# Kernel tuning notes

Measured on AMD Instinct MI355X. Metric: run time of the kernel, lower is better.

The kernel has to match this reference:

```python
import jax, jax.numpy as jnp
import numpy as np

VOCAB, EMB, HID, OUT = 32000, 512, 1024, 512
B, S = 64, 256


def setup_inputs() -> dict:
    key = jax.random.key(0)
    ks = jax.random.split(key, 16)
    def xavier(k, shape):
        bound = np.sqrt(6.0 / (shape[0] + shape[1]))
        return jax.random.uniform(k, shape, jnp.float32, -bound, bound)
    return {
        "tokens": jax.random.randint(ks[0], (B, S), 0, VOCAB),
        "emb": jax.random.normal(ks[1], (VOCAB, EMB), jnp.float32) * 0.02,
        "W_xi": xavier(ks[2], (EMB, HID)),
        "W_xf": xavier(ks[3], (EMB, HID)),
        "W_xo": xavier(ks[4], (EMB, HID)),
        "W_xc": xavier(ks[5], (EMB, HID)),
        "W_hi": xavier(ks[6], (HID, HID)),
        "W_hf": xavier(ks[7], (HID, HID)),
        "W_ho": xavier(ks[8], (HID, HID)),
        "W_hc": xavier(ks[9], (HID, HID)),
        "W_hy": xavier(ks[10], (HID, OUT)),
        "b_i": jnp.zeros((HID,), jnp.float32),
        "b_f": jnp.zeros((HID,), jnp.float32),
        "b_o": jnp.zeros((HID,), jnp.float32),
        "b_c": jnp.zeros((HID,), jnp.float32),
        "b_hy": jnp.zeros((OUT,), jnp.float32),
    }


def reference(tokens, emb, W_xi, W_xf, W_xo, W_xc, W_hi, W_hf, W_ho, W_hc,
              W_hy, b_i, b_f, b_o, b_c, b_hy):
    # Embedding lookup for all timesteps (dropout is identity at inference).
    x = emb[tokens]  # [B, S, E]
    # Precompute input-to-gate projections in one batched GEMM per gate.
    gx_i = jnp.einsum('bse,eh->bsh', x, W_xi) + b_i
    gx_f = jnp.einsum('bse,eh->bsh', x, W_xf) + b_f
    gx_o = jnp.einsum('bse,eh->bsh', x, W_xo) + b_o
    gx_c = jnp.einsum('bse,eh->bsh', x, W_xc) + b_c
    # Time-major stacked gates: [S, B, 4, H]
    g = jnp.stack([gx_i, gx_f, gx_o, gx_c], axis=2).transpose(1, 0, 2, 3)

    h0 = jnp.zeros((tokens.shape[0], W_hi.shape[0]), x.dtype)
    c0 = jnp.zeros_like(h0)

    def step(carry, g_t):
        h, c = carry
        i = jax.nn.sigmoid(g_t[:, 0] + h @ W_hi)
        f = jax.nn.sigmoid(g_t[:, 1] + h @ W_hf)
        o = jax.nn.sigmoid(g_t[:, 2] + h @ W_ho)
        cc = jnp.tanh(g_t[:, 3] + h @ W_hc)
        c = f * c + i * cc
        h = o * jnp.tanh(c)
        return (h, c), None

    (h, c), _ = jax.lax.scan(step, (h0, c0), g)
    return h @ W_hy + b_hy  # [B, OUT]
```

## Files before the change

### kernel.cpp

```cpp
#include <hip/hip_runtime.h>
#include <hip/hip_bf16.h>

#define EMBN   512
#define HIDN   1024
#define OUTN   512
#define BBN    64
#define SSN    256
#define NBLK   256
#define PSTR   20

typedef __attribute__((ext_vector_type(8))) short bf16x8;
typedef __attribute__((ext_vector_type(4))) float f32x4;
typedef __attribute__((ext_vector_type(4))) int int4v;
typedef unsigned short us;
typedef unsigned long long ull;

static __device__ __forceinline__ us f2bf(float x) {
  unsigned int u = __float_as_uint(x);
  unsigned int r = (u + 0x7fffu + ((u >> 16) & 1u)) >> 16;
  return (us)r;
}
static __device__ __forceinline__ float bf2f(us u) {
  unsigned int v = ((unsigned int)u) << 16;
  return __uint_as_float(v);
}

__global__ void pack_w(const float* __restrict__ wxi, const float* __restrict__ wxf,
                       const float* __restrict__ wxo, const float* __restrict__ wxc,
                       const float* __restrict__ whi, const float* __restrict__ whf,
                       const float* __restrict__ who, const float* __restrict__ whc,
                       us* __restrict__ Whip, us* __restrict__ Wlop) {
  int idx = blockIdx.x * 256 + threadIdx.x;
  int lane = idx & 63;
  int kt   = (idx >> 6) % 48;
  int j    = idx / (48 * 64);
  int q = lane & 15, g = q >> 2, r = q & 3;
  int hd = 4 * j + r;
  int kb = kt * 32 + ((lane >> 4) << 3);
  const float* wx = (g == 0) ? wxi : (g == 1) ? wxf : (g == 2) ? wxo : wxc;
  const float* wh = (g == 0) ? whi : (g == 1) ? whf : (g == 2) ? who : whc;
  long obase = (long)idx * 8;
  #pragma unroll
  for (int jj = 0; jj < 8; ++jj) {
    int k = kb + jj;
    float v = (k < EMBN) ? wx[(long)k * HIDN + hd] : wh[(long)(k - EMBN) * HIDN + hd];
    us hi = f2bf(v);
    us lo = f2bf(v - bf2f(hi));
    Whip[obase + jj] = hi;
    Wlop[obase + jj] = lo;
  }
}

__global__ void pack_x(const int* __restrict__ tokens, const float* __restrict__ emb,
                       us* __restrict__ Xhi, us* __restrict__ Xlo) {
  int idx = blockIdx.x * 256 + threadIdx.x;
  int k = idx & 511;
  int b = (idx >> 9) & 63;
  int t = idx >> 15;
  int tok = tokens[b * SSN + t];
  float v = emb[(long)tok * EMBN + k];
  us hi = f2bf(v);
  Xhi[idx] = hi;
  Xlo[idx] = f2bf(v - bf2f(hi));
}

#define XISS(A, c) { _Pragma("unroll") for (int q = 0; q < 4; ++q) { \
      A[2*q]   = *(const bf16x8*)(xh + (((c)*4 + q) << 5)); \
      A[2*q+1] = *(const bf16x8*)(xl + (((c)*4 + q) << 5)); } }
#define XCON(A, c) { _Pragma("unroll") for (int q = 0; q < 4; ++q) { \
      const int kt = (c)*4 + q; \
      bf16x8 w0 = *(const bf16x8*)(WHi + (kt << 9) + (lane << 3)); \
      bf16x8 w1 = *(const bf16x8*)(WLo + (kt << 9) + (lane << 3)); \
      accA = __builtin_amdgcn_mfma_f32_16x16x32_bf16(w0, A[2*q],   accA, 0, 0, 0); \
      accB = __builtin_amdgcn_mfma_f32_16x16x32_bf16(w0, A[2*q+1], accB, 0, 0, 0); \
      accC = __builtin_amdgcn_mfma_f32_16x16x32_bf16(w1, A[2*q],   accC, 0, 0, 0); } }
#define HISS(A, c) { _Pragma("unroll") for (int q = 0; q < 4; ++q) { \
      A[2*q]   = *(const bf16x8*)(hh + (((c)*4 + q) << 5)); \
      A[2*q+1] = *(const bf16x8*)(hl + (((c)*4 + q) << 5)); } }
#define HCON(A, c) { _Pragma("unroll") for (int q = 0; q < 4; ++q) { \
      const int kt = 16 + (c)*4 + q; \
      bf16x8 w0 = *(const bf16x8*)(WHi + (kt << 9) + (lane << 3)); \
      bf16x8 w1 = *(const bf16x8*)(WLo + (kt << 9) + (lane << 3)); \
      accA = __builtin_amdgcn_mfma_f32_16x16x32_bf16(w0, A[2*q],   accA, 0, 0, 0); \
      accB = __builtin_amdgcn_mfma_f32_16x16x32_bf16(w0, A[2*q+1], accB, 0, 0, 0); \
      accC = __builtin_amdgcn_mfma_f32_16x16x32_bf16(w1, A[2*q],   accC, 0, 0, 0); } }

__launch_bounds__(256, 1)
__global__ void lstm_persist(const us* __restrict__ Whip, const us* __restrict__ Wlop,
                             const us* __restrict__ Xhi, const us* __restrict__ Xlo,
                             us* Hhi, us* Hlo, float* hfin, int* flags,
                             const float* __restrict__ biP, const float* __restrict__ bfP,
                             const float* __restrict__ boP, const float* __restrict__ bcP,
                             int K) {
  extern __shared__ char smem[];
  us* WHi = (us*)smem;
  us* WLo = WHi + 24576;
  float* preact = (float*)(smem + 98304);

  const int j = blockIdx.x, tid = threadIdx.x;
  const int wv = tid >> 6, lane = tid & 63;
  const int Km = K - 1;
  const bool ROT = (K != 256);

  {
    const uint4* shi = (const uint4*)(Whip + (long)j * 24576);
    const uint4* slo = (const uint4*)(Wlop + (long)j * 24576);
    uint4* dhi = (uint4*)WHi;
    uint4* dlo = (uint4*)WLo;
    for (int i = tid; i < 3072; i += 256) { dhi[i] = shi[i]; dlo[i] = slo[i]; }
  }
  const int gb = tid >> 2, gr = tid & 3;
  const float bi_r = biP[4 * j + gr], bf_r = bfP[4 * j + gr];
  const float bo_r = boP[4 * j + gr], bc_r = bcP[4 * j + gr];
  float c_reg = 0.f;

  const int mrow = (wv << 4) + (lane & 15);
  const int kj = (lane >> 4) << 3;
  const int p0 = (lane >> 4) << 2;
  int* const flagsP = flags + (wv << 8);
  __syncthreads();

  f32x4 accA = {0.f, 0.f, 0.f, 0.f};
  f32x4 accB = {0.f, 0.f, 0.f, 0.f};
  f32x4 accC = {0.f, 0.f, 0.f, 0.f};

  {
    const us* xh = Xhi + (mrow << 9) + kj;
    const us* xl = Xlo + (mrow << 9) + kj;
    bf16x8 XA[8], XB[8];
    XISS(XA, 0) XISS(XB, 1)
    __builtin_amdgcn_sched_barrier(0);
    XCON(XA, 0) XISS(XA, 2)
    __builtin_amdgcn_sched_barrier(0);
    XCON(XB, 1) XISS(XB, 3)
    __builtin_amdgcn_sched_barrier(0);
    XCON(XA, 2) XCON(XB, 3)
  }

  #pragma unroll 1
  for (int t = 0; t < SSN; ++t) {
    if (t > 0) {
      if (ROT && (t & Km) == 0)
        __builtin_amdgcn_fence(__ATOMIC_ACQUIRE, "agent");

      {
        const int* fp = flagsP + (lane << 2);
        int4v f;
        for (;;) {
          asm volatile("global_load_dwordx4 %0, %1, off sc0 sc1\n\t"
                       "s_waitcnt vmcnt(0)"
                       : "=&v"(f) : "v"(fp) : "memory");
          if (!__any((f.x < t) | (f.y < t) | (f.z < t) | (f.w < t))) break;
          __builtin_amdgcn_s_sleep(2);
        }
      }

      const int cur = t & Km;
      const us* hh = Hhi + (((long)cur * BBN + mrow) << 10) + kj;
      const us* hl = Hlo + (((long)cur * BBN + mrow) << 10) + kj;
      bf16x8 HA[8], HB[8], HC[8], HD[8];
      HISS(HA, 0) HISS(HB, 1) HISS(HC, 2) HISS(HD, 3)
      __builtin_amdgcn_sched_barrier(0);
      HCON(HA, 0) HISS(HA, 4)
      __builtin_amdgcn_sched_barrier(0);
      HCON(HB, 1) HISS(HB, 5)
      __builtin_amdgcn_sched_barrier(0);
      HCON(HC, 2) HISS(HC, 6)
      __builtin_amdgcn_sched_barrier(0);
      HCON(HD, 3) HISS(HD, 7)
      __builtin_amdgcn_sched_barrier(0);
      HCON(HA, 4) HCON(HB, 5) HCON(HC, 6) HCON(HD, 7)
    }

    {
      f32x4 acc = accA + accB;
      acc = acc + accC;
      *(f32x4*)(preact + mrow * PSTR + p0) = acc;
    }

    {
      float pi = preact[gb * PSTR + gr]      + bi_r;
      float pf = preact[gb * PSTR + 4 + gr]  + bf_r;
      float po = preact[gb * PSTR + 8 + gr]  + bo_r;
      float pc = preact[gb * PSTR + 12 + gr] + bc_r;
      float vi = 1.f / (1.f + expf(-pi));
      float vf = 1.f / (1.f + expf(-pf));
      float vo = 1.f / (1.f + expf(-po));
      float vc = tanhf(pc);
      c_reg = vf * c_reg + vi * vc;
      float h = vo * tanhf(c_reg);

      if (t == SSN - 1) {
        hfin[(gb << 10) + 4 * j + gr] = h;
      } else {
        us hh_ = f2bf(h);
        us hl_ = f2bf(h - bf2f(hh_));
        unsigned int hpair = (unsigned int)hh_ | ((unsigned int)hl_ << 16);
        const int base = lane & ~3;
        unsigned int g0 = (unsigned int)__shfl((int)hpair, base);
        unsigned int g1 = (unsigned int)__shfl((int)hpair, base + 1);
        unsigned int g2 = (unsigned int)__shfl((int)hpair, base + 2);
        unsigned int g3 = (unsigned int)__shfl((int)hpair, base + 3);
        unsigned int hi01 = (g0 & 0xffffu) | (g1 << 16);
        unsigned int hi23 = (g2 & 0xffffu) | (g3 << 16);
        unsigned int lo01 = (g0 >> 16)     | (g1 & 0xffff0000u);
        unsigned int lo23 = (g2 >> 16)     | (g3 & 0xffff0000u);
        ull hiq = ((ull)hi23 << 32) | (ull)hi01;
        ull loq = ((ull)lo23 << 32) | (ull)lo01;

        const long nxt = (long)((t + 1) & Km);
        if (gr == 0) {
          __hip_atomic_store((ull*)(Hhi + ((nxt * BBN + gb) << 10) + 4 * j), hiq,
                             __ATOMIC_RELAXED, __HIP_MEMORY_SCOPE_AGENT);
          __hip_atomic_store((ull*)(Hlo + ((nxt * BBN + gb) << 10) + 4 * j), loq,
                             __ATOMIC_RELAXED, __HIP_MEMORY_SCOPE_AGENT);
        }

        const us* xh = Xhi + ((long)(t + 1) << 15) + (mrow << 9) + kj;
        const us* xl = Xlo + ((long)(t + 1) << 15) + (mrow << 9) + kj;
        bf16x8 XA[8], XB[8];
        XISS(XA, 0) XISS(XB, 1)
        asm volatile("s_waitcnt vmcnt(0)" ::: "memory");
        if (lane == 0)
          __hip_atomic_store(&flagsP[j], t + 1,
                             __ATOMIC_RELAXED, __HIP_MEMORY_SCOPE_AGENT);
        __builtin_amdgcn_sched_barrier(0);
        accA = {0.f, 0.f, 0.f, 0.f};
        accB = {0.f, 0.f, 0.f, 0.f};
        accC = {0.f, 0.f, 0.f, 0.f};
        XCON(XA, 0) XISS(XA, 2)
        __builtin_amdgcn_sched_barrier(0);
        XCON(XB, 1) XISS(XB, 3)
        __builtin_amdgcn_sched_barrier(0);
        XCON(XA, 2) XCON(XB, 3)
      }
    }
  }
}

__global__ void out_gemm(const float* __restrict__ hfin, const float* __restrict__ Why,
                         const float* __restrict__ bhy, float* __restrict__ out) {
  int b = blockIdx.x, n = threadIdx.x;
  const float* h = hfin + (b << 10);
  float acc = 0.f;
  #pragma unroll 8
  for (int k = 0; k < HIDN; ++k) acc = fmaf(h[k], Why[(k << 9) + n], acc);
  out[(b << 9) + n] = acc + bhy[n];
}

extern "C" void kernel_launch(void* const* d_in, const int* in_sizes, int n_in,
                              void* d_out, int out_size, void* d_ws, size_t ws_size,
                              hipStream_t stream) {
  const int*   tokens = (const int*)d_in[0];
  const float* emb    = (const float*)d_in[1];
  const float* Wxi    = (const float*)d_in[2];
  const float* Wxf    = (const float*)d_in[3];
  const float* Wxo    = (const float*)d_in[4];
  const float* Wxc    = (const float*)d_in[5];
  const float* Whi_   = (const float*)d_in[6];
  const float* Whf    = (const float*)d_in[7];
  const float* Who    = (const float*)d_in[8];
  const float* Whc    = (const float*)d_in[9];
  const float* Why    = (const float*)d_in[10];
  const float* bi     = (const float*)d_in[11];
  const float* bfv    = (const float*)d_in[12];
  const float* bo     = (const float*)d_in[13];
  const float* bc     = (const float*)d_in[14];
  const float* bhy    = (const float*)d_in[15];
  float* outp = (float*)d_out;

  char* ws = (char*)d_ws;
  size_t off = 0;
  auto carve = [&](size_t bytes) -> void* {
    void* p = ws + off;
    off += (bytes + 255) & ~(size_t)255;
    return p;
  };
  us*    Whip = (us*)carve(12582912);
  us*    Wlop = (us*)carve(12582912);
  us*    Xhi  = (us*)carve(16777216);
  us*    Xlo  = (us*)carve(16777216);
  float* hfin = (float*)carve(262144);
  int*   flags = (int*)carve(4096);

  size_t rem = (ws_size > off) ? (ws_size - off) : 0;
  int K = 256;
  while (K > 8 && (size_t)2 * (size_t)K * 131072 + 512 > rem) K >>= 1;
  if ((size_t)2 * (size_t)K * 131072 + 512 > rem) {
    (void)hipMemsetAsync(d_out, 0, (size_t)out_size * 4, stream);
    return;
  }
  us* Hhi = (us*)carve((size_t)K * 131072);
  us* Hlo = (us*)carve((size_t)K * 131072);

  (void)hipMemsetAsync(flags, 0, 4096, stream);

  pack_w<<<3072, 256, 0, stream>>>(Wxi, Wxf, Wxo, Wxc, Whi_, Whf, Who, Whc, Whip, Wlop);
  pack_x<<<32768, 256, 0, stream>>>(tokens, emb, Xhi, Xlo);

  (void)hipFuncSetAttribute((const void*)lstm_persist,
                            hipFuncAttributeMaxDynamicSharedMemorySize, 103424);
  lstm_persist<<<NBLK, 256, 103424, stream>>>(Whip, Wlop, Xhi, Xlo, Hhi, Hlo,
                                              hfin, flags, bi, bfv, bo, bc, K);
  out_gemm<<<BBN, OUTN, 0, stream>>>(hfin, Why, bhy, outp);
}
```

Baseline: 2.821 ms.

## Replace per-step flag polling with sentinel-tagged hidden-state data polling

Removes the separate flags array and its spin loop. Consumers now load the hidden-state tiles directly and re-poll only when they see an all-ones sentinel, which the hidden buffers are memset to before launch. Producers no longer need a vmcnt wait plus a flag store after writing h. This saves a round trip on the recurrent critical path. It relies on a valid bf16 pair never equalling 0xFFFFFFFF (NaN pattern), and on the max check over lanes x and z catching partially written tiles. When the buffer ring wraps, slots are re-marked with sentinels, which adds extra stores and a wait.

```diff
diff --git a/kernel.cpp b/kernel.cpp
--- a/kernel.cpp
+++ b/kernel.cpp
@@ -11,7 +11,7 @@
 
 typedef __attribute__((ext_vector_type(8))) short bf16x8;
 typedef __attribute__((ext_vector_type(4))) float f32x4;
-typedef __attribute__((ext_vector_type(4))) int int4v;
+typedef __attribute__((ext_vector_type(4))) unsigned int u32x4;
 typedef unsigned short us;
 typedef unsigned long long ull;
 
@@ -74,9 +74,39 @@
       accA = __builtin_amdgcn_mfma_f32_16x16x32_bf16(w0, A[2*q],   accA, 0, 0, 0); \
       accB = __builtin_amdgcn_mfma_f32_16x16x32_bf16(w0, A[2*q+1], accB, 0, 0, 0); \
       accC = __builtin_amdgcn_mfma_f32_16x16x32_bf16(w1, A[2*q],   accC, 0, 0, 0); } }
-#define HISS(A, c) { _Pragma("unroll") for (int q = 0; q < 4; ++q) { \
-      A[2*q]   = *(const bf16x8*)(hh + (((c)*4 + q) << 5)); \
-      A[2*q+1] = *(const bf16x8*)(hl + (((c)*4 + q) << 5)); } }
+
+#define HLD(A, S, c) { _Pragma("unroll") for (int q = 0; q < 4; ++q) { \
+      const int ct = (c)*4 + q; \
+      u32x4 rh = *(const u32x4*)(hh + (ct << 5)); \
+      u32x4 rl = *(const u32x4*)(hl + (ct << 5)); \
+      A[2*q]   = *(bf16x8*)&rh; \
+      A[2*q+1] = *(bf16x8*)&rl; \
+      unsigned int m0 = rh.x > rh.z ? rh.x : rh.z; \
+      unsigned int m1 = rl.x > rl.z ? rl.x : rl.z; \
+      S[q] = m0 > m1 ? m0 : m1; } }
+#define HRLD(A, S, c) { _Pragma("unroll") for (int q = 0; q < 4; ++q) { \
+      const int ct = (c)*4 + q; \
+      u32x4 rh, rl; \
+      asm volatile("global_load_dwordx4 %0, %2, off sc0 sc1\n\t" \
+                   "global_load_dwordx4 %1, %3, off sc0 sc1\n\t" \
+                   "s_waitcnt vmcnt(0)" \
+                   : "=&v"(rh), "=&v"(rl) \
+                   : "v"(hh + (ct << 5)), "v"(hl + (ct << 5)) : "memory"); \
+      A[2*q]   = *(bf16x8*)&rh; \
+      A[2*q+1] = *(bf16x8*)&rl; \
+      unsigned int m0 = rh.x > rh.z ? rh.x : rh.z; \
+      unsigned int m1 = rl.x > rl.z ? rl.x : rl.z; \
+      S[q] = m0 > m1 ? m0 : m1; } }
+#define HCHK(A, S, c) { \
+      unsigned int m01 = S[0] > S[1] ? S[0] : S[1]; \
+      unsigned int m23 = S[2] > S[3] ? S[2] : S[3]; \
+      unsigned int mm  = m01 > m23 ? m01 : m23; \
+      while (__builtin_expect(__any(mm == 0xffffffffu), 0)) { \
+        __builtin_amdgcn_s_sleep(1); \
+        HRLD(A, S, c) \
+        m01 = S[0] > S[1] ? S[0] : S[1]; \
+        m23 = S[2] > S[3] ? S[2] : S[3]; \
+        mm  = m01 > m23 ? m01 : m23; } }
 #define HCON(A, c) { _Pragma("unroll") for (int q = 0; q < 4; ++q) { \
       const int kt = 16 + (c)*4 + q; \
       bf16x8 w0 = *(const bf16x8*)(WHi + (kt << 9) + (lane << 3)); \
@@ -88,7 +118,7 @@
 __launch_bounds__(256, 1)
 __global__ void lstm_persist(const us* __restrict__ Whip, const us* __restrict__ Wlop,
                              const us* __restrict__ Xhi, const us* __restrict__ Xlo,
-                             us* Hhi, us* Hlo, float* hfin, int* flags,
+                             us* Hhi, us* Hlo, float* hfin,
                              const float* __restrict__ biP, const float* __restrict__ bfP,
                              const float* __restrict__ boP, const float* __restrict__ bcP,
                              int K) {
@@ -100,7 +130,7 @@
   const int j = blockIdx.x, tid = threadIdx.x;
   const int wv = tid >> 6, lane = tid & 63;
   const int Km = K - 1;
-  const bool ROT = (K != 256);
+  const bool SENT = (K != 256);
 
   {
     const uint4* shi = (const uint4*)(Whip + (long)j * 24576);
@@ -117,7 +147,6 @@
   const int mrow = (wv << 4) + (lane & 15);
   const int kj = (lane >> 4) << 3;
   const int p0 = (lane >> 4) << 2;
-  int* const flagsP = flags + (wv << 8);
   __syncthreads();
 
   f32x4 accA = {0.f, 0.f, 0.f, 0.f};
@@ -140,36 +169,36 @@
   #pragma unroll 1
   for (int t = 0; t < SSN; ++t) {
     if (t > 0) {
-      if (ROT && (t & Km) == 0)
+      if (SENT && (t & Km) == 0)
         __builtin_amdgcn_fence(__ATOMIC_ACQUIRE, "agent");
-
-      {
-        const int* fp = flagsP + (lane << 2);
-        int4v f;
-        for (;;) {
-          asm volatile("global_load_dwordx4 %0, %1, off sc0 sc1\n\t"
-                       "s_waitcnt vmcnt(0)"
-                       : "=&v"(f) : "v"(fp) : "memory");
-          if (!__any((f.x < t) | (f.y < t) | (f.z < t) | (f.w < t))) break;
-          __builtin_amdgcn_s_sleep(2);
-        }
-      }
 
       const int cur = t & Km;
       const us* hh = Hhi + (((long)cur * BBN + mrow) << 10) + kj;
       const us* hl = Hlo + (((long)cur * BBN + mrow) << 10) + kj;
       bf16x8 HA[8], HB[8], HC[8], HD[8];
-      HISS(HA, 0) HISS(HB, 1) HISS(HC, 2) HISS(HD, 3)
-      __builtin_amdgcn_sched_barrier(0);
-      HCON(HA, 0) HISS(HA, 4)
-      __builtin_amdgcn_sched_barrier(0);
-      HCON(HB, 1) HISS(HB, 5)
-      __builtin_amdgcn_sched_barrier(0);
-      HCON(HC, 2) HISS(HC, 6)
-      __builtin_amdgcn_sched_barrier(0);
-      HCON(HD, 3) HISS(HD, 7)
-      __builtin_amdgcn_sched_barrier(0);
-      HCON(HA, 4) HCON(HB, 5) HCON(HC, 6) HCON(HD, 7)
+      unsigned int SA[4], SB_[4], SC[4], SD[4];
+      HLD(HA, SA, 0) HLD(HB, SB_, 1) HLD(HC, SC, 2) HLD(HD, SD, 3)
+      __builtin_amdgcn_sched_barrier(0);
+      HCHK(HA, SA, 0)  HCON(HA, 0) HLD(HA, SA, 4)
+      __builtin_amdgcn_sched_barrier(0);
+      HCHK(HB, SB_, 1) HCON(HB, 1) HLD(HB, SB_, 5)
+      __builtin_amdgcn_sched_barrier(0);
+      HCHK(HC, SC, 2)  HCON(HC, 2) HLD(HC, SC, 6)
+      __builtin_amdgcn_sched_barrier(0);
+      HCHK(HD, SD, 3)  HCON(HD, 3) HLD(HD, SD, 7)
+      __builtin_amdgcn_sched_barrier(0);
+      HCHK(HA, SA, 4)  HCON(HA, 4)
+      HCHK(HB, SB_, 5) HCON(HB, 5)
+      HCHK(HC, SC, 6)  HCON(HC, 6)
+      HCHK(HD, SD, 7)  HCON(HD, 7)
+
+      if (SENT && t + 2 >= K && t + 2 < SSN && gr == 0) {
+        const long snt = (long)((t + 2) & Km);
+        __hip_atomic_store((ull*)(Hhi + ((snt * BBN + gb) << 10) + 4 * j), ~0ull,
+                           __ATOMIC_RELAXED, __HIP_MEMORY_SCOPE_AGENT);
+        __hip_atomic_store((ull*)(Hlo + ((snt * BBN + gb) << 10) + 4 * j), ~0ull,
+                           __ATOMIC_RELAXED, __HIP_MEMORY_SCOPE_AGENT);
+      }
     }
 
     {
@@ -208,6 +237,8 @@
         ull hiq = ((ull)hi23 << 32) | (ull)hi01;
         ull loq = ((ull)lo23 << 32) | (ull)lo01;
 
+        if (SENT) asm volatile("s_waitcnt vmcnt(0)" ::: "memory");
+
         const long nxt = (long)((t + 1) & Km);
         if (gr == 0) {
           __hip_atomic_store((ull*)(Hhi + ((nxt * BBN + gb) << 10) + 4 * j), hiq,
@@ -220,10 +251,6 @@
         const us* xl = Xlo + ((long)(t + 1) << 15) + (mrow << 9) + kj;
         bf16x8 XA[8], XB[8];
         XISS(XA, 0) XISS(XB, 1)
-        asm volatile("s_waitcnt vmcnt(0)" ::: "memory");
-        if (lane == 0)
-          __hip_atomic_store(&flagsP[j], t + 1,
-                             __ATOMIC_RELAXED, __HIP_MEMORY_SCOPE_AGENT);
         __builtin_amdgcn_sched_barrier(0);
         accA = {0.f, 0.f, 0.f, 0.f};
         accB = {0.f, 0.f, 0.f, 0.f};
@@ -281,7 +308,6 @@
   us*    Xhi  = (us*)carve(16777216);
   us*    Xlo  = (us*)carve(16777216);
   float* hfin = (float*)carve(262144);
-  int*   flags = (int*)carve(4096);
 
   size_t rem = (ws_size > off) ? (ws_size - off) : 0;
   int K = 256;
@@ -293,7 +319,8 @@
   us* Hhi = (us*)carve((size_t)K * 131072);
   us* Hlo = (us*)carve((size_t)K * 131072);
 
-  (void)hipMemsetAsync(flags, 0, 4096, stream);
+  (void)hipMemsetAsync(Hhi, 0xFF, (size_t)K * 131072, stream);
+  (void)hipMemsetAsync(Hlo, 0xFF, (size_t)K * 131072, stream);
 
   pack_w<<<3072, 256, 0, stream>>>(Wxi, Wxf, Wxo, Wxc, Whi_, Whf, Who, Whc, Whip, Wlop);
   pack_x<<<32768, 256, 0, stream>>>(tokens, emb, Xhi, Xlo);
@@ -301,6 +328,6 @@
   (void)hipFuncSetAttribute((const void*)lstm_persist,
                             hipFuncAttributeMaxDynamicSharedMemorySize, 103424);
   lstm_persist<<<NBLK, 256, 103424, stream>>>(Whip, Wlop, Xhi, Xlo, Hhi, Hlo,
-                                              hfin, flags, bi, bfv, bo, bc, K);
+                                              hfin, bi, bfv, bo, bc, K);
   out_gemm<<<BBN, OUTN, 0, stream>>>(hfin, Why, bhy, outp);
 }
```

New measurement: 4.793 ms. +69.9%, slower.

## Split each persistent block's K reduction across two wave halves with LDS handoff

Applied to the files above, without the earlier changes.

The persistent LSTM kernel now launches 512 threads per block and pairs waves so each pair splits the x and h K-dimension in half. Partial preactivations go to two LDS buffers, joined by a workgroup-scoped spin flag, and only the s=0 wave does the gate math and publishes h. The x-projection for step t is no longer prefetched during step t-1; it now runs at the start of each step, before the cross-block flag wait. The aim is to halve per-wave MFMA and load latency on the serial recurrence critical path. The cost is an intra-block spin wait, doubled register and wave pressure, and a shorter s_sleep in the global poll.

```diff
diff --git a/kernel.cpp b/kernel.cpp
--- a/kernel.cpp
+++ b/kernel.cpp
@@ -64,28 +64,18 @@
   Xlo[idx] = f2bf(v - bf2f(hi));
 }
 
-#define XISS(A, c) { _Pragma("unroll") for (int q = 0; q < 4; ++q) { \
-      A[2*q]   = *(const bf16x8*)(xh + (((c)*4 + q) << 5)); \
-      A[2*q+1] = *(const bf16x8*)(xl + (((c)*4 + q) << 5)); } }
-#define XCON(A, c) { _Pragma("unroll") for (int q = 0; q < 4; ++q) { \
-      const int kt = (c)*4 + q; \
+#define GISS(A, P, PL, c) { _Pragma("unroll") for (int q = 0; q < 4; ++q) { \
+      A[2*q]   = *(const bf16x8*)((P)  + (((c)*4 + q) << 5)); \
+      A[2*q+1] = *(const bf16x8*)((PL) + (((c)*4 + q) << 5)); } }
+#define GCON(A, c, kb) { _Pragma("unroll") for (int q = 0; q < 4; ++q) { \
+      const int kt = (kb) + (c)*4 + q; \
       bf16x8 w0 = *(const bf16x8*)(WHi + (kt << 9) + (lane << 3)); \
       bf16x8 w1 = *(const bf16x8*)(WLo + (kt << 9) + (lane << 3)); \
       accA = __builtin_amdgcn_mfma_f32_16x16x32_bf16(w0, A[2*q],   accA, 0, 0, 0); \
       accB = __builtin_amdgcn_mfma_f32_16x16x32_bf16(w0, A[2*q+1], accB, 0, 0, 0); \
       accC = __builtin_amdgcn_mfma_f32_16x16x32_bf16(w1, A[2*q],   accC, 0, 0, 0); } }
-#define HISS(A, c) { _Pragma("unroll") for (int q = 0; q < 4; ++q) { \
-      A[2*q]   = *(const bf16x8*)(hh + (((c)*4 + q) << 5)); \
-      A[2*q+1] = *(const bf16x8*)(hl + (((c)*4 + q) << 5)); } }
-#define HCON(A, c) { _Pragma("unroll") for (int q = 0; q < 4; ++q) { \
-      const int kt = 16 + (c)*4 + q; \
-      bf16x8 w0 = *(const bf16x8*)(WHi + (kt << 9) + (lane << 3)); \
-      bf16x8 w1 = *(const bf16x8*)(WLo + (kt << 9) + (lane << 3)); \
-      accA = __builtin_amdgcn_mfma_f32_16x16x32_bf16(w0, A[2*q],   accA, 0, 0, 0); \
-      accB = __builtin_amdgcn_mfma_f32_16x16x32_bf16(w0, A[2*q+1], accB, 0, 0, 0); \
-      accC = __builtin_amdgcn_mfma_f32_16x16x32_bf16(w1, A[2*q],   accC, 0, 0, 0); } }
-
-__launch_bounds__(256, 1)
+
+__launch_bounds__(512, 2)
 __global__ void lstm_persist(const us* __restrict__ Whip, const us* __restrict__ Wlop,
                              const us* __restrict__ Xhi, const us* __restrict__ Xlo,
                              us* Hhi, us* Hlo, float* hfin, int* flags,
@@ -95,10 +85,13 @@
   extern __shared__ char smem[];
   us* WHi = (us*)smem;
   us* WLo = WHi + 24576;
-  float* preact = (float*)(smem + 98304);
+  float* pre0 = (float*)(smem + 98304);
+  float* pre1 = (float*)(smem + 103424);
+  int*   lfl  = (int*)(smem + 108544);
 
   const int j = blockIdx.x, tid = threadIdx.x;
   const int wv = tid >> 6, lane = tid & 63;
+  const int p = wv >> 1, s = wv & 1;
   const int Km = K - 1;
   const bool ROT = (K != 256);
 
@@ -107,38 +100,38 @@
     const uint4* slo = (const uint4*)(Wlop + (long)j * 24576);
     uint4* dhi = (uint4*)WHi;
     uint4* dlo = (uint4*)WLo;
-    for (int i = tid; i < 3072; i += 256) { dhi[i] = shi[i]; dlo[i] = slo[i]; }
-  }
-  const int gb = tid >> 2, gr = tid & 3;
+    for (int i = tid; i < 3072; i += 512) { dhi[i] = shi[i]; dlo[i] = slo[i]; }
+  }
+  if (tid < 4) lfl[tid] = 0;
+
+  const int gr = lane & 3;
   const float bi_r = biP[4 * j + gr], bf_r = bfP[4 * j + gr];
   const float bo_r = boP[4 * j + gr], bc_r = bcP[4 * j + gr];
   float c_reg = 0.f;
 
-  const int mrow = (wv << 4) + (lane & 15);
+  const int mrow = (p << 4) + (lane & 15);
   const int kj = (lane >> 4) << 3;
   const int p0 = (lane >> 4) << 2;
-  int* const flagsP = flags + (wv << 8);
+  const int xk0 = s << 3;
+  const int hk0 = 16 + (s << 4);
+  int* const flagsP = flags + (p << 8);
   __syncthreads();
-
-  f32x4 accA = {0.f, 0.f, 0.f, 0.f};
-  f32x4 accB = {0.f, 0.f, 0.f, 0.f};
-  f32x4 accC = {0.f, 0.f, 0.f, 0.f};
-
-  {
-    const us* xh = Xhi + (mrow << 9) + kj;
-    const us* xl = Xlo + (mrow << 9) + kj;
-    bf16x8 XA[8], XB[8];
-    XISS(XA, 0) XISS(XB, 1)
-    __builtin_amdgcn_sched_barrier(0);
-    XCON(XA, 0) XISS(XA, 2)
-    __builtin_amdgcn_sched_barrier(0);
-    XCON(XB, 1) XISS(XB, 3)
-    __builtin_amdgcn_sched_barrier(0);
-    XCON(XA, 2) XCON(XB, 3)
-  }
 
   #pragma unroll 1
   for (int t = 0; t < SSN; ++t) {
+    f32x4 accA = {0.f, 0.f, 0.f, 0.f};
+    f32x4 accB = {0.f, 0.f, 0.f, 0.f};
+    f32x4 accC = {0.f, 0.f, 0.f, 0.f};
+
+    {
+      const us* xh = Xhi + ((long)t << 15) + (mrow << 9) + (xk0 << 5) + kj;
+      const us* xl = Xlo + ((long)t << 15) + (mrow << 9) + (xk0 << 5) + kj;
+      bf16x8 XA[8], XB[8];
+      GISS(XA, xh, xl, 0) GISS(XB, xh, xl, 1)
+      __builtin_amdgcn_sched_barrier(0);
+      GCON(XA, 0, xk0) GCON(XB, 1, xk0)
+    }
+
     if (t > 0) {
       if (ROT && (t & Km) == 0)
         __builtin_amdgcn_fence(__ATOMIC_ACQUIRE, "agent");
@@ -151,38 +144,38 @@
                        "s_waitcnt vmcnt(0)"
                        : "=&v"(f) : "v"(fp) : "memory");
           if (!__any((f.x < t) | (f.y < t) | (f.z < t) | (f.w < t))) break;
-          __builtin_amdgcn_s_sleep(2);
+          __builtin_amdgcn_s_sleep(1);
         }
       }
 
       const int cur = t & Km;
-      const us* hh = Hhi + (((long)cur * BBN + mrow) << 10) + kj;
-      const us* hl = Hlo + (((long)cur * BBN + mrow) << 10) + kj;
+      const us* hh = Hhi + (((long)cur * BBN + mrow) << 10) + (s << 9) + kj;
+      const us* hl = Hlo + (((long)cur * BBN + mrow) << 10) + (s << 9) + kj;
       bf16x8 HA[8], HB[8], HC[8], HD[8];
-      HISS(HA, 0) HISS(HB, 1) HISS(HC, 2) HISS(HD, 3)
+      GISS(HA, hh, hl, 0) GISS(HB, hh, hl, 1) GISS(HC, hh, hl, 2) GISS(HD, hh, hl, 3)
       __builtin_amdgcn_sched_barrier(0);
-      HCON(HA, 0) HISS(HA, 4)
+      GCON(HA, 0, hk0) GCON(HB, 1, hk0) GCON(HC, 2, hk0) GCON(HD, 3, hk0)
+    }
+
+    f32x4 acc = accA + accB;
+    acc = acc + accC;
+
+    if (s) {
+      *(f32x4*)(pre1 + mrow * PSTR + p0) = acc;
+      asm volatile("s_waitcnt lgkmcnt(0)" ::: "memory");
+      __hip_atomic_store(&lfl[p], t + 1, __ATOMIC_RELAXED, __HIP_MEMORY_SCOPE_WORKGROUP);
+    } else {
+      *(f32x4*)(pre0 + mrow * PSTR + p0) = acc;
+      while (__hip_atomic_load(&lfl[p], __ATOMIC_RELAXED, __HIP_MEMORY_SCOPE_WORKGROUP) < t + 1) {}
       __builtin_amdgcn_sched_barrier(0);
-      HCON(HB, 1) HISS(HB, 5)
-      __builtin_amdgcn_sched_barrier(0);
-      HCON(HC, 2) HISS(HC, 6)
-      __builtin_amdgcn_sched_barrier(0);
-      HCON(HD, 3) HISS(HD, 7)
-      __builtin_amdgcn_sched_barrier(0);
-      HCON(HA, 4) HCON(HB, 5) HCON(HC, 6) HCON(HD, 7)
-    }
-
-    {
-      f32x4 acc = accA + accB;
-      acc = acc + accC;
-      *(f32x4*)(preact + mrow * PSTR + p0) = acc;
-    }
-
-    {
-      float pi = preact[gb * PSTR + gr]      + bi_r;
-      float pf = preact[gb * PSTR + 4 + gr]  + bf_r;
-      float po = preact[gb * PSTR + 8 + gr]  + bo_r;
-      float pc = preact[gb * PSTR + 12 + gr] + bc_r;
+
+      const int row = (p << 4) + (lane >> 2);
+      const float* q0 = pre0 + row * PSTR;
+      const float* q1 = pre1 + row * PSTR;
+      float pi = q0[gr]      + q1[gr]      + bi_r;
+      float pf = q0[4 + gr]  + q1[4 + gr]  + bf_r;
+      float po = q0[8 + gr]  + q1[8 + gr]  + bo_r;
+      float pc = q0[12 + gr] + q1[12 + gr] + bc_r;
       float vi = 1.f / (1.f + expf(-pi));
       float vf = 1.f / (1.f + expf(-pf));
       float vo = 1.f / (1.f + expf(-po));
@@ -191,7 +184,7 @@
       float h = vo * tanhf(c_reg);
 
       if (t == SSN - 1) {
-        hfin[(gb << 10) + 4 * j + gr] = h;
+        hfin[(row << 10) + 4 * j + gr] = h;
       } else {
         us hh_ = f2bf(h);
         us hl_ = f2bf(h - bf2f(hh_));
@@ -210,29 +203,15 @@
 
         const long nxt = (long)((t + 1) & Km);
         if (gr == 0) {
-          __hip_atomic_store((ull*)(Hhi + ((nxt * BBN + gb) << 10) + 4 * j), hiq,
+          __hip_atomic_store((ull*)(Hhi + ((nxt * BBN + row) << 10) + 4 * j), hiq,
                              __ATOMIC_RELAXED, __HIP_MEMORY_SCOPE_AGENT);
-          __hip_atomic_store((ull*)(Hlo + ((nxt * BBN + gb) << 10) + 4 * j), loq,
+          __hip_atomic_store((ull*)(Hlo + ((nxt * BBN + row) << 10) + 4 * j), loq,
                              __ATOMIC_RELAXED, __HIP_MEMORY_SCOPE_AGENT);
         }
-
-        const us* xh = Xhi + ((long)(t + 1) << 15) + (mrow << 9) + kj;
-        const us* xl = Xlo + ((long)(t + 1) << 15) + (mrow << 9) + kj;
-        bf16x8 XA[8], XB[8];
-        XISS(XA, 0) XISS(XB, 1)
         asm volatile("s_waitcnt vmcnt(0)" ::: "memory");
         if (lane == 0)
           __hip_atomic_store(&flagsP[j], t + 1,
                              __ATOMIC_RELAXED, __HIP_MEMORY_SCOPE_AGENT);
-        __builtin_amdgcn_sched_barrier(0);
-        accA = {0.f, 0.f, 0.f, 0.f};
-        accB = {0.f, 0.f, 0.f, 0.f};
-        accC = {0.f, 0.f, 0.f, 0.f};
-        XCON(XA, 0) XISS(XA, 2)
-        __builtin_amdgcn_sched_barrier(0);
-        XCON(XB, 1) XISS(XB, 3)
-        __builtin_amdgcn_sched_barrier(0);
-        XCON(XA, 2) XCON(XB, 3)
       }
     }
   }
@@ -299,8 +278,8 @@
   pack_x<<<32768, 256, 0, stream>>>(tokens, emb, Xhi, Xlo);
 
   (void)hipFuncSetAttribute((const void*)lstm_persist,
-                            hipFuncAttributeMaxDynamicSharedMemorySize, 103424);
-  lstm_persist<<<NBLK, 256, 103424, stream>>>(Whip, Wlop, Xhi, Xlo, Hhi, Hlo,
+                            hipFuncAttributeMaxDynamicSharedMemorySize, 108560);
+  lstm_persist<<<NBLK, 512, 108560, stream>>>(Whip, Wlop, Xhi, Xlo, Hhi, Hlo,
                                               hfin, flags, bi, bfv, bo, bc, K);
   out_gemm<<<BBN, OUTN, 0, stream>>>(hfin, Why, bhy, outp);
 }
```

Measured after the change: 4.578 ms. 1.62x slower.

## Halve persistent LSTM blocks, each handling two hidden slices with weights split across LDS and registers

Applied to the files above, without the earlier changes.

The persistent recurrent kernel now runs on 128 blocks instead of 256. Each block computes two 4-column hidden slices: one slice's weights sit fully in shared memory, and the other's are split between 44 register-resident bf16x8 fragments and shared memory. This halves the number of blocks that publish and poll per-step flags, which is meant to cut cross-block synchronisation overhead in the time loop. In exchange each block does twice the MFMA work per step and holds very high register and LDS pressure, with a risk of spills.

```diff
diff --git a/kernel.cpp b/kernel.cpp
--- a/kernel.cpp
+++ b/kernel.cpp
@@ -6,8 +6,8 @@
 #define OUTN   512
 #define BBN    64
 #define SSN    256
-#define NBLK   256
-#define PSTR   20
+#define NBLK   128
+#define PST2   36
 
 typedef __attribute__((ext_vector_type(8))) short bf16x8;
 typedef __attribute__((ext_vector_type(4))) float f32x4;
@@ -33,9 +33,9 @@
   int idx = blockIdx.x * 256 + threadIdx.x;
   int lane = idx & 63;
   int kt   = (idx >> 6) % 48;
-  int j    = idx / (48 * 64);
+  int v    = idx / (48 * 64);
   int q = lane & 15, g = q >> 2, r = q & 3;
-  int hd = 4 * j + r;
+  int hd = 4 * v + r;
   int kb = kt * 32 + ((lane >> 4) << 3);
   const float* wx = (g == 0) ? wxi : (g == 1) ? wxf : (g == 2) ? wxo : wxc;
   const float* wh = (g == 0) ? whi : (g == 1) ? whf : (g == 2) ? who : whc;
@@ -43,9 +43,9 @@
   #pragma unroll
   for (int jj = 0; jj < 8; ++jj) {
     int k = kb + jj;
-    float v = (k < EMBN) ? wx[(long)k * HIDN + hd] : wh[(long)(k - EMBN) * HIDN + hd];
-    us hi = f2bf(v);
-    us lo = f2bf(v - bf2f(hi));
+    float val = (k < EMBN) ? wx[(long)k * HIDN + hd] : wh[(long)(k - EMBN) * HIDN + hd];
+    us hi = f2bf(val);
+    us lo = f2bf(val - bf2f(hi));
     Whip[obase + jj] = hi;
     Wlop[obase + jj] = lo;
   }
@@ -67,23 +67,35 @@
 #define XISS(A, c) { _Pragma("unroll") for (int q = 0; q < 4; ++q) { \
       A[2*q]   = *(const bf16x8*)(xh + (((c)*4 + q) << 5)); \
       A[2*q+1] = *(const bf16x8*)(xl + (((c)*4 + q) << 5)); } }
-#define XCON(A, c) { _Pragma("unroll") for (int q = 0; q < 4; ++q) { \
-      const int kt = (c)*4 + q; \
-      bf16x8 w0 = *(const bf16x8*)(WHi + (kt << 9) + (lane << 3)); \
-      bf16x8 w1 = *(const bf16x8*)(WLo + (kt << 9) + (lane << 3)); \
-      accA = __builtin_amdgcn_mfma_f32_16x16x32_bf16(w0, A[2*q],   accA, 0, 0, 0); \
-      accB = __builtin_amdgcn_mfma_f32_16x16x32_bf16(w0, A[2*q+1], accB, 0, 0, 0); \
-      accC = __builtin_amdgcn_mfma_f32_16x16x32_bf16(w1, A[2*q],   accC, 0, 0, 0); } }
 #define HISS(A, c) { _Pragma("unroll") for (int q = 0; q < 4; ++q) { \
       A[2*q]   = *(const bf16x8*)(hh + (((c)*4 + q) << 5)); \
       A[2*q+1] = *(const bf16x8*)(hl + (((c)*4 + q) << 5)); } }
-#define HCON(A, c) { _Pragma("unroll") for (int q = 0; q < 4; ++q) { \
+
+#define XCON2(A, c) { _Pragma("unroll") for (int q = 0; q < 4; ++q) { \
+      const int kt = (c)*4 + q; \
+      bf16x8 w0h = *(const bf16x8*)(W0Hi + (kt << 9) + (lane << 3)); \
+      bf16x8 w0l = *(const bf16x8*)(W0Lo + (kt << 9) + (lane << 3)); \
+      a0A = __builtin_amdgcn_mfma_f32_16x16x32_bf16(w0h, A[2*q],   a0A, 0, 0, 0); \
+      a0B = __builtin_amdgcn_mfma_f32_16x16x32_bf16(w0h, A[2*q+1], a0B, 0, 0, 0); \
+      a0C = __builtin_amdgcn_mfma_f32_16x16x32_bf16(w0l, A[2*q],   a0C, 0, 0, 0); \
+      bf16x8 w1h = RW[2*kt], w1l = RW[2*kt+1]; \
+      a1A = __builtin_amdgcn_mfma_f32_16x16x32_bf16(w1h, A[2*q],   a1A, 0, 0, 0); \
+      a1B = __builtin_amdgcn_mfma_f32_16x16x32_bf16(w1h, A[2*q+1], a1B, 0, 0, 0); \
+      a1C = __builtin_amdgcn_mfma_f32_16x16x32_bf16(w1l, A[2*q],   a1C, 0, 0, 0); } }
+#define HCON2(A, c) { _Pragma("unroll") for (int q = 0; q < 4; ++q) { \
       const int kt = 16 + (c)*4 + q; \
-      bf16x8 w0 = *(const bf16x8*)(WHi + (kt << 9) + (lane << 3)); \
-      bf16x8 w1 = *(const bf16x8*)(WLo + (kt << 9) + (lane << 3)); \
-      accA = __builtin_amdgcn_mfma_f32_16x16x32_bf16(w0, A[2*q],   accA, 0, 0, 0); \
-      accB = __builtin_amdgcn_mfma_f32_16x16x32_bf16(w0, A[2*q+1], accB, 0, 0, 0); \
-      accC = __builtin_amdgcn_mfma_f32_16x16x32_bf16(w1, A[2*q],   accC, 0, 0, 0); } }
+      bf16x8 w0h = *(const bf16x8*)(W0Hi + (kt << 9) + (lane << 3)); \
+      bf16x8 w0l = *(const bf16x8*)(W0Lo + (kt << 9) + (lane << 3)); \
+      a0A = __builtin_amdgcn_mfma_f32_16x16x32_bf16(w0h, A[2*q],   a0A, 0, 0, 0); \
+      a0B = __builtin_amdgcn_mfma_f32_16x16x32_bf16(w0h, A[2*q+1], a0B, 0, 0, 0); \
+      a0C = __builtin_amdgcn_mfma_f32_16x16x32_bf16(w0l, A[2*q],   a0C, 0, 0, 0); \
+      bf16x8 w1h, w1l; \
+      if (kt < 22) { w1h = RW[2*kt]; w1l = RW[2*kt+1]; } \
+      else { w1h = *(const bf16x8*)(W1Hi + ((kt - 22) << 9) + (lane << 3)); \
+             w1l = *(const bf16x8*)(W1Lo + ((kt - 22) << 9) + (lane << 3)); } \
+      a1A = __builtin_amdgcn_mfma_f32_16x16x32_bf16(w1h, A[2*q],   a1A, 0, 0, 0); \
+      a1B = __builtin_amdgcn_mfma_f32_16x16x32_bf16(w1h, A[2*q+1], a1B, 0, 0, 0); \
+      a1C = __builtin_amdgcn_mfma_f32_16x16x32_bf16(w1l, A[2*q],   a1C, 0, 0, 0); } }
 
 __launch_bounds__(256, 1)
 __global__ void lstm_persist(const us* __restrict__ Whip, const us* __restrict__ Wlop,
@@ -93,36 +105,56 @@
                              const float* __restrict__ boP, const float* __restrict__ bcP,
                              int K) {
   extern __shared__ char smem[];
-  us* WHi = (us*)smem;
-  us* WLo = WHi + 24576;
-  float* preact = (float*)(smem + 98304);
+  us* W0Hi = (us*)smem;
+  us* W0Lo = (us*)(smem + 49152);
+  us* W1Hi = (us*)(smem + 98304);
+  us* W1Lo = (us*)(smem + 124928);
+  float* preact = (float*)(smem + 151552);
 
   const int j = blockIdx.x, tid = threadIdx.x;
   const int wv = tid >> 6, lane = tid & 63;
   const int Km = K - 1;
   const bool ROT = (K != 256);
+  const long v0 = 2 * j, v1 = 2 * j + 1;
 
   {
-    const uint4* shi = (const uint4*)(Whip + (long)j * 24576);
-    const uint4* slo = (const uint4*)(Wlop + (long)j * 24576);
-    uint4* dhi = (uint4*)WHi;
-    uint4* dlo = (uint4*)WLo;
-    for (int i = tid; i < 3072; i += 256) { dhi[i] = shi[i]; dlo[i] = slo[i]; }
-  }
+    const uint4* s0h = (const uint4*)(Whip + v0 * 24576);
+    const uint4* s0l = (const uint4*)(Wlop + v0 * 24576);
+    uint4* d0h = (uint4*)W0Hi;
+    uint4* d0l = (uint4*)W0Lo;
+    for (int i = tid; i < 3072; i += 256) { d0h[i] = s0h[i]; d0l[i] = s0l[i]; }
+    const uint4* s1h = (const uint4*)(Whip + v1 * 24576 + 11264);
+    const uint4* s1l = (const uint4*)(Wlop + v1 * 24576 + 11264);
+    uint4* d1h = (uint4*)W1Hi;
+    uint4* d1l = (uint4*)W1Lo;
+    for (int i = tid; i < 1664; i += 256) { d1h[i] = s1h[i]; d1l[i] = s1l[i]; }
+  }
+  bf16x8 RW[44];
+  {
+    const us* rwh = Whip + v1 * 24576 + (lane << 3);
+    const us* rwl = Wlop + v1 * 24576 + (lane << 3);
+    #pragma unroll
+    for (int i = 0; i < 22; ++i) {
+      RW[2*i]   = *(const bf16x8*)(rwh + (i << 9));
+      RW[2*i+1] = *(const bf16x8*)(rwl + (i << 9));
+    }
+  }
+
   const int gb = tid >> 2, gr = tid & 3;
-  const float bi_r = biP[4 * j + gr], bf_r = bfP[4 * j + gr];
-  const float bo_r = boP[4 * j + gr], bc_r = bcP[4 * j + gr];
-  float c_reg = 0.f;
+  const float bi_0 = biP[8*j + gr],     bf_0 = bfP[8*j + gr];
+  const float bo_0 = boP[8*j + gr],     bc_0 = bcP[8*j + gr];
+  const float bi_1 = biP[8*j + 4 + gr], bf_1 = bfP[8*j + 4 + gr];
+  const float bo_1 = boP[8*j + 4 + gr], bc_1 = bcP[8*j + 4 + gr];
+  float c0 = 0.f, c1 = 0.f;
 
   const int mrow = (wv << 4) + (lane & 15);
   const int kj = (lane >> 4) << 3;
   const int p0 = (lane >> 4) << 2;
-  int* const flagsP = flags + (wv << 8);
+  int* const flagsP = flags + (wv << 7);
   __syncthreads();
 
-  f32x4 accA = {0.f, 0.f, 0.f, 0.f};
-  f32x4 accB = {0.f, 0.f, 0.f, 0.f};
-  f32x4 accC = {0.f, 0.f, 0.f, 0.f};
+  f32x4 a0A = {0.f,0.f,0.f,0.f}, a0B = {0.f,0.f,0.f,0.f}, a0C = {0.f,0.f,0.f,0.f};
+  f32x4 a1A = {0.f,0.f,0.f,0.f}, a1B = {0.f,0.f,0.f,0.f}, a1C = {0.f,0.f,0.f,0.f};
 
   {
     const us* xh = Xhi + (mrow << 9) + kj;
@@ -130,11 +162,11 @@
     bf16x8 XA[8], XB[8];
     XISS(XA, 0) XISS(XB, 1)
     __builtin_amdgcn_sched_barrier(0);
-    XCON(XA, 0) XISS(XA, 2)
+    XCON2(XA, 0) XISS(XA, 2)
     __builtin_amdgcn_sched_barrier(0);
-    XCON(XB, 1) XISS(XB, 3)
+    XCON2(XB, 1) XISS(XB, 3)
     __builtin_amdgcn_sched_barrier(0);
-    XCON(XA, 2) XCON(XB, 3)
+    XCON2(XA, 2) XCON2(XB, 3)
   }
 
   #pragma unroll 1
@@ -144,7 +176,7 @@
         __builtin_amdgcn_fence(__ATOMIC_ACQUIRE, "agent");
 
       {
-        const int* fp = flagsP + (lane << 2);
+        const int* fp = flagsP + ((lane & 31) << 2);
         int4v f;
         for (;;) {
           asm volatile("global_load_dwordx4 %0, %1, off sc0 sc1\n\t"
@@ -161,59 +193,71 @@
       bf16x8 HA[8], HB[8], HC[8], HD[8];
       HISS(HA, 0) HISS(HB, 1) HISS(HC, 2) HISS(HD, 3)
       __builtin_amdgcn_sched_barrier(0);
-      HCON(HA, 0) HISS(HA, 4)
-      __builtin_amdgcn_sched_barrier(0);
-      HCON(HB, 1) HISS(HB, 5)
-      __builtin_amdgcn_sched_barrier(0);
-      HCON(HC, 2) HISS(HC, 6)
-      __builtin_amdgcn_sched_barrier(0);
-      HCON(HD, 3) HISS(HD, 7)
-      __builtin_amdgcn_sched_barrier(0);
-      HCON(HA, 4) HCON(HB, 5) HCON(HC, 6) HCON(HD, 7)
+      HCON2(HA, 0) HISS(HA, 4)
+      __builtin_amdgcn_sched_barrier(0);
+      HCON2(HB, 1) HISS(HB, 5)
+      __builtin_amdgcn_sched_barrier(0);
+      HCON2(HC, 2) HISS(HC, 6)
+      __builtin_amdgcn_sched_barrier(0);
+      HCON2(HD, 3) HISS(HD, 7)
+      __builtin_amdgcn_sched_barrier(0);
+      HCON2(HA, 4) HCON2(HB, 5) HCON2(HC, 6) HCON2(HD, 7)
     }
 
     {
-      f32x4 acc = accA + accB;
-      acc = acc + accC;
-      *(f32x4*)(preact + mrow * PSTR + p0) = acc;
+      f32x4 s0 = a0A + a0B; s0 = s0 + a0C;
+      f32x4 s1 = a1A + a1B; s1 = s1 + a1C;
+      *(f32x4*)(preact + mrow * PST2 + p0)      = s0;
+      *(f32x4*)(preact + mrow * PST2 + 16 + p0) = s1;
     }
 
     {
-      float pi = preact[gb * PSTR + gr]      + bi_r;
-      float pf = preact[gb * PSTR + 4 + gr]  + bf_r;
-      float po = preact[gb * PSTR + 8 + gr]  + bo_r;
-      float pc = preact[gb * PSTR + 12 + gr] + bc_r;
-      float vi = 1.f / (1.f + expf(-pi));
-      float vf = 1.f / (1.f + expf(-pf));
-      float vo = 1.f / (1.f + expf(-po));
-      float vc = tanhf(pc);
-      c_reg = vf * c_reg + vi * vc;
-      float h = vo * tanhf(c_reg);
+      const float* pr = preact + gb * PST2;
+      float pi0 = pr[gr]      + bi_0, pf0 = pr[4 + gr]  + bf_0;
+      float po0 = pr[8 + gr]  + bo_0, pc0 = pr[12 + gr] + bc_0;
+      float pi1 = pr[16 + gr] + bi_1, pf1 = pr[20 + gr] + bf_1;
+      float po1 = pr[24 + gr] + bo_1, pc1 = pr[28 + gr] + bc_1;
+      float vi0 = 1.f / (1.f + expf(-pi0)), vf0 = 1.f / (1.f + expf(-pf0));
+      float vo0 = 1.f / (1.f + expf(-po0)), vc0 = tanhf(pc0);
+      float vi1 = 1.f / (1.f + expf(-pi1)), vf1 = 1.f / (1.f + expf(-pf1));
+      float vo1 = 1.f / (1.f + expf(-po1)), vc1 = tanhf(pc1);
+      c0 = vf0 * c0 + vi0 * vc0;
+      c1 = vf1 * c1 + vi1 * vc1;
+      float h0 = vo0 * tanhf(c0);
+      float h1 = vo1 * tanhf(c1);
 
       if (t == SSN - 1) {
-        hfin[(gb << 10) + 4 * j + gr] = h;
+        hfin[(gb << 10) + 8*j + gr]     = h0;
+        hfin[(gb << 10) + 8*j + 4 + gr] = h1;
       } else {
-        us hh_ = f2bf(h);
-        us hl_ = f2bf(h - bf2f(hh_));
-        unsigned int hpair = (unsigned int)hh_ | ((unsigned int)hl_ << 16);
+        us h0h = f2bf(h0), h0l = f2bf(h0 - bf2f(h0h));
+        us h1h = f2bf(h1), h1l = f2bf(h1 - bf2f(h1h));
+        unsigned int hp0 = (unsigned int)h0h | ((unsigned int)h0l << 16);
+        unsigned int hp1 = (unsigned int)h1h | ((unsigned int)h1l << 16);
         const int base = lane & ~3;
-        unsigned int g0 = (unsigned int)__shfl((int)hpair, base);
-        unsigned int g1 = (unsigned int)__shfl((int)hpair, base + 1);
-        unsigned int g2 = (unsigned int)__shfl((int)hpair, base + 2);
-        unsigned int g3 = (unsigned int)__shfl((int)hpair, base + 3);
-        unsigned int hi01 = (g0 & 0xffffu) | (g1 << 16);
-        unsigned int hi23 = (g2 & 0xffffu) | (g3 << 16);
-        unsigned int lo01 = (g0 >> 16)     | (g1 & 0xffff0000u);
-        unsigned int lo23 = (g2 >> 16)     | (g3 & 0xffff0000u);
-        ull hiq = ((ull)hi23 << 32) | (ull)hi01;
-        ull loq = ((ull)lo23 << 32) | (ull)lo01;
+        unsigned int a0 = (unsigned int)__shfl((int)hp0, base);
+        unsigned int a1 = (unsigned int)__shfl((int)hp0, base + 1);
+        unsigned int a2 = (unsigned int)__shfl((int)hp0, base + 2);
+        unsigned int a3 = (unsigned int)__shfl((int)hp0, base + 3);
+        unsigned int b0 = (unsigned int)__shfl((int)hp1, base);
+        unsigned int b1 = (unsigned int)__shfl((int)hp1, base + 1);
+        unsigned int b2 = (unsigned int)__shfl((int)hp1, base + 2);
+        unsigned int b3 = (unsigned int)__shfl((int)hp1, base + 3);
+        unsigned int hi01 = (a0 & 0xffffu) | (a1 << 16), hi23 = (a2 & 0xffffu) | (a3 << 16);
+        unsigned int hi45 = (b0 & 0xffffu) | (b1 << 16), hi67 = (b2 & 0xffffu) | (b3 << 16);
+        unsigned int lo01 = (a0 >> 16) | (a1 & 0xffff0000u), lo23 = (a2 >> 16) | (a3 & 0xffff0000u);
+        unsigned int lo45 = (b0 >> 16) | (b1 & 0xffff0000u), lo67 = (b2 >> 16) | (b3 & 0xffff0000u);
+        ull hiq0 = ((ull)hi23 << 32) | hi01, hiq1 = ((ull)hi67 << 32) | hi45;
+        ull loq0 = ((ull)lo23 << 32) | lo01, loq1 = ((ull)lo67 << 32) | lo45;
 
         const long nxt = (long)((t + 1) & Km);
         if (gr == 0) {
-          __hip_atomic_store((ull*)(Hhi + ((nxt * BBN + gb) << 10) + 4 * j), hiq,
-                             __ATOMIC_RELAXED, __HIP_MEMORY_SCOPE_AGENT);
-          __hip_atomic_store((ull*)(Hlo + ((nxt * BBN + gb) << 10) + 4 * j), loq,
-                             __ATOMIC_RELAXED, __HIP_MEMORY_SCOPE_AGENT);
+          us* ph = Hhi + ((nxt * BBN + gb) << 10) + 8*j;
+          us* pl = Hlo + ((nxt * BBN + gb) << 10) + 8*j;
+          __hip_atomic_store((ull*)ph,       hiq0, __ATOMIC_RELAXED, __HIP_MEMORY_SCOPE_AGENT);
+          __hip_atomic_store((ull*)(ph + 4), hiq1, __ATOMIC_RELAXED, __HIP_MEMORY_SCOPE_AGENT);
+          __hip_atomic_store((ull*)pl,       loq0, __ATOMIC_RELAXED, __HIP_MEMORY_SCOPE_AGENT);
+          __hip_atomic_store((ull*)(pl + 4), loq1, __ATOMIC_RELAXED, __HIP_MEMORY_SCOPE_AGENT);
         }
 
         const us* xh = Xhi + ((long)(t + 1) << 15) + (mrow << 9) + kj;
@@ -225,14 +269,13 @@
           __hip_atomic_store(&flagsP[j], t + 1,
                              __ATOMIC_RELAXED, __HIP_MEMORY_SCOPE_AGENT);
         __builtin_amdgcn_sched_barrier(0);
-        accA = {0.f, 0.f, 0.f, 0.f};
-        accB = {0.f, 0.f, 0.f, 0.f};
-        accC = {0.f, 0.f, 0.f, 0.f};
-        XCON(XA, 0) XISS(XA, 2)
+        a0A = {0.f,0.f,0.f,0.f}; a0B = {0.f,0.f,0.f,0.f}; a0C = {0.f,0.f,0.f,0.f};
+        a1A = {0.f,0.f,0.f,0.f}; a1B = {0.f,0.f,0.f,0.f}; a1C = {0.f,0.f,0.f,0.f};
+        XCON2(XA, 0) XISS(XA, 2)
         __builtin_amdgcn_sched_barrier(0);
-        XCON(XB, 1) XISS(XB, 3)
+        XCON2(XB, 1) XISS(XB, 3)
         __builtin_amdgcn_sched_barrier(0);
-        XCON(XA, 2) XCON(XB, 3)
+        XCON2(XA, 2) XCON2(XB, 3)
       }
     }
   }
@@ -281,7 +324,7 @@
   us*    Xhi  = (us*)carve(16777216);
   us*    Xlo  = (us*)carve(16777216);
   float* hfin = (float*)carve(262144);
-  int*   flags = (int*)carve(4096);
+  int*   flags = (int*)carve(2048);
 
   size_t rem = (ws_size > off) ? (ws_size - off) : 0;
   int K = 256;
@@ -293,14 +336,14 @@
   us* Hhi = (us*)carve((size_t)K * 131072);
   us* Hlo = (us*)carve((size_t)K * 131072);
 
-  (void)hipMemsetAsync(flags, 0, 4096, stream);
+  (void)hipMemsetAsync(flags, 0, 2048, stream);
 
   pack_w<<<3072, 256, 0, stream>>>(Wxi, Wxf, Wxo, Wxc, Whi_, Whf, Who, Whc, Whip, Wlop);
   pack_x<<<32768, 256, 0, stream>>>(tokens, emb, Xhi, Xlo);
 
   (void)hipFuncSetAttribute((const void*)lstm_persist,
-                            hipFuncAttributeMaxDynamicSharedMemorySize, 103424);
-  lstm_persist<<<NBLK, 256, 103424, stream>>>(Whip, Wlop, Xhi, Xlo, Hhi, Hlo,
+                            hipFuncAttributeMaxDynamicSharedMemorySize, 160768);
+  lstm_persist<<<NBLK, 256, 160768, stream>>>(Whip, Wlop, Xhi, Xlo, Hhi, Hlo,
                                               hfin, flags, bi, bfv, bo, bc, K);
   out_gemm<<<BBN, OUTN, 0, stream>>>(hfin, Why, bhy, outp);
 }
```

Result: slower. 2.922 ms (+3.6%).
